# Kernel optimization log

Measured on AMD Instinct MI355X. Metric: run time of the kernel, lower is better.

Reference implementation:

```python
import jax, jax.numpy as jnp
import numpy as np

NEG_SLOPE = 0.2  # PyG GATConv default LeakyReLU negative slope


def gat_conv(x, src, dst, W, att_src, att_dst, bias, heads, out_ch, concat):
    """PyG-style GATConv (eval mode, self-loops already appended to src/dst)."""
    n = x.shape[0]
    xh = (x @ W).reshape(n, heads, out_ch)          # [N, H, C]
    a_src = jnp.sum(xh * att_src, axis=-1)          # [N, H]
    a_dst = jnp.sum(xh * att_dst, axis=-1)          # [N, H]
    e = jax.nn.leaky_relu(a_src[src] + a_dst[dst], NEG_SLOPE)  # [E, H]
    # segment softmax over edges grouped by destination node
    m = jax.ops.segment_max(e, dst, num_segments=n)
    m = jnp.where(jnp.isfinite(m), m, 0.0)
    ex = jnp.exp(e - m[dst])
    denom = jax.ops.segment_sum(ex, dst, num_segments=n)
    alpha = ex / (denom[dst] + 1e-16)               # [E, H]
    msg = xh[src] * alpha[..., None]                # [E, H, C]
    out = jax.ops.segment_sum(msg, dst, num_segments=n)  # [N, H, C]
    out = out.reshape(n, heads * out_ch) if concat else out.mean(axis=1)
    return out + bias


def setup_inputs() -> dict:
    key = jax.random.key(0)
    ks = jax.random.split(key, 10)
    N, E, IN, OUT = 50000, 600000, 128, 64
    H1, C1 = 2, 2 * OUT   # conv1: heads=2, out=2*out_channels, concat -> 4*OUT
    H2, C2 = 1, OUT       # conv2: heads=1, concat=False
    s = 0.05
    return {
        "x": jax.random.normal(ks[0], (N, IN), dtype=jnp.float32),
        "edge_index": jax.random.randint(ks[1], (2, E), 0, N, dtype=jnp.int64),
        "W1": jax.random.normal(ks[2], (IN, H1 * C1), dtype=jnp.float32) * s,
        "att_src1": jax.random.normal(ks[3], (H1, C1), dtype=jnp.float32) * s,
        "att_dst1": jax.random.normal(ks[4], (H1, C1), dtype=jnp.float32) * s,
        "b1": jnp.zeros((H1 * C1,), dtype=jnp.float32),
        "W2": jax.random.normal(ks[5], (H1 * C1, H2 * C2), dtype=jnp.float32) * s,
        "att_src2": jax.random.normal(ks[6], (H2, C2), dtype=jnp.float32) * s,
        "att_dst2": jax.random.normal(ks[7], (H2, C2), dtype=jnp.float32) * s,
        "b2": jnp.zeros((C2,), dtype=jnp.float32),
    }


def reference(x, edge_index, W1, att_src1, att_dst1, b1, W2, att_src2, att_dst2, b2):
    n = x.shape[0]
    loop = jnp.arange(n, dtype=edge_index.dtype)
    src = jnp.concatenate([edge_index[0], loop])  # add_self_loops=True
    dst = jnp.concatenate([edge_index[1], loop])
    z = gat_conv(x, src, dst, W1, att_src1, att_dst1, b1, heads=2, out_ch=128, concat=True)
    z = jax.nn.relu(z)
    z = gat_conv(z, src, dst, W2, att_src2, att_dst2, b2, heads=1, out_ch=64, concat=False)
    # decode: dot product over original edge_index (no self loops)
    val = jnp.sum(z[edge_index[0]] * z[edge_index[1]], axis=-1)
    return val.reshape(-1)
```

## Files before the change

### kernel.cpp

```cpp
#include <hip/hip_runtime.h>
#include <math.h>

#define IN_F 128
#define F1 256
#define H1 2
#define F2 64
#define NEG 0.2f

typedef _Float16 f16x8 __attribute__((ext_vector_type(8)));
typedef _Float16 f16x4 __attribute__((ext_vector_type(4)));
typedef float f32x4 __attribute__((ext_vector_type(4)));

__global__ __launch_bounds__(256) void gemm12_fused(
    const _Float16* __restrict__ Gh, const _Float16* __restrict__ Gl,
    const _Float16* __restrict__ Wth, const _Float16* __restrict__ Wtl,
    const float* __restrict__ b1,
    const _Float16* __restrict__ W2th, const _Float16* __restrict__ W2tl,
    const float* __restrict__ as2, const float* __restrict__ ad2,
    float* __restrict__ xh2, float* __restrict__ a_src, float* __restrict__ a_dst,
    int N)
{
    __shared__ _Float16 FRGh[32 * 64 * 8];
    __shared__ _Float16 FRGl[32 * 64 * 8];
    __shared__ _Float16 Zh[64 * 256];
    __shared__ _Float16 Zl[64 * 256];

    int t = threadIdx.x;
    int wave = t >> 6, lane = t & 63;
    int quad = lane >> 4, l4 = lane & 15;
    int rt = blockIdx.x * 4 + wave;
    bool active = (rt * 16 < N);
    long mrow = (long)rt * 16 + l4;

    #pragma unroll 1
    for (int h = 0; h < 2; ++h) {
        const _Float16* wsh = Wth + (long)h * 128 * IN_F;
        const _Float16* wsl = Wtl + (long)h * 128 * IN_F;
        #pragma unroll
        for (int p = 0; p < 8; ++p) {
            int fs = p * 256 + t;
            int fl = fs & 63;
            int slot = fs >> 6;
            int ct = slot >> 2, ks = slot & 3;
            int col = ct * 16 + (fl & 15);
            int koff = ks * 32 + (fl >> 4) * 8;
            *(f16x8*)&FRGh[fs * 8] = *(const f16x8*)&wsh[(long)col * IN_F + koff];
            *(f16x8*)&FRGl[fs * 8] = *(const f16x8*)&wsl[(long)col * IN_F + koff];
        }
        __syncthreads();

        if (active) {
            const _Float16* gh = Gh + mrow * F1 + h * 128 + quad * 8;
            const _Float16* gl = Gl + mrow * F1 + h * 128 + quad * 8;
            f16x8 ah[4], al[4];
            #pragma unroll
            for (int ks = 0; ks < 4; ++ks) {
                ah[ks] = *(const f16x8*)(gh + ks * 32);
                al[ks] = *(const f16x8*)(gl + ks * 32);
            }
            f32x4 acc[8];
            #pragma unroll
            for (int ct = 0; ct < 8; ++ct) acc[ct] = (f32x4){0.f, 0.f, 0.f, 0.f};
            #pragma unroll
            for (int ks = 0; ks < 4; ++ks) {
                #pragma unroll
                for (int ct = 0; ct < 8; ++ct) {
                    f16x8 bh = *(const f16x8*)&FRGh[((ct * 4 + ks) * 64 + lane) * 8];
                    f16x8 bl = *(const f16x8*)&FRGl[((ct * 4 + ks) * 64 + lane) * 8];
                    acc[ct] = __builtin_amdgcn_mfma_f32_16x16x32_f16(ah[ks], bh, acc[ct], 0, 0, 0);
                    acc[ct] = __builtin_amdgcn_mfma_f32_16x16x32_f16(al[ks], bh, acc[ct], 0, 0, 0);
                    acc[ct] = __builtin_amdgcn_mfma_f32_16x16x32_f16(ah[ks], bl, acc[ct], 0, 0, 0);
                }
            }
            #pragma unroll
            for (int ct = 0; ct < 8; ++ct) {
                int col = h * 128 + ct * 16 + l4;
                float b1c = b1[col];
                #pragma unroll
                for (int i = 0; i < 4; ++i) {
                    int row = wave * 16 + quad * 4 + i;
                    float v = fmaxf(acc[ct][i] + b1c, 0.f);
                    _Float16 hi = (_Float16)v;
                    int e = (row * 256 + col) ^ ((row & 7) << 3);
                    Zh[e] = hi;
                    Zl[e] = (_Float16)(v - (float)hi);
                }
            }
        }
        __syncthreads();
    }

    #pragma unroll
    for (int p = 0; p < 8; ++p) {
        int fs = p * 256 + t;
        int fl = fs & 63;
        int slot = fs >> 6;
        int ct = slot >> 3, ks = slot & 7;
        int col = ct * 16 + (fl & 15);
        int koff = ks * 32 + (fl >> 4) * 8;
        *(f16x8*)&FRGh[fs * 8] = *(const f16x8*)&W2th[(long)col * F1 + koff];
        *(f16x8*)&FRGl[fs * 8] = *(const f16x8*)&W2tl[(long)col * F1 + koff];
    }
    __syncthreads();

    if (!active) return;
    {
        int row = wave * 16 + l4;
        int swz = (row & 7) << 3;
        f16x8 ah[8], al[8];
        #pragma unroll
        for (int ks = 0; ks < 8; ++ks) {
            int e = (row * 256 + (quad * 8 + ks * 32)) ^ swz;
            ah[ks] = *(const f16x8*)&Zh[e];
            al[ks] = *(const f16x8*)&Zl[e];
        }
        f32x4 acc[4];
        #pragma unroll
        for (int ct = 0; ct < 4; ++ct) acc[ct] = (f32x4){0.f, 0.f, 0.f, 0.f};
        #pragma unroll
        for (int ks = 0; ks < 8; ++ks) {
            #pragma unroll
            for (int ct = 0; ct < 4; ++ct) {
                f16x8 bh = *(const f16x8*)&FRGh[((ct * 8 + ks) * 64 + lane) * 8];
                f16x8 bl = *(const f16x8*)&FRGl[((ct * 8 + ks) * 64 + lane) * 8];
                acc[ct] = __builtin_amdgcn_mfma_f32_16x16x32_f16(ah[ks], bh, acc[ct], 0, 0, 0);
                acc[ct] = __builtin_amdgcn_mfma_f32_16x16x32_f16(al[ks], bh, acc[ct], 0, 0, 0);
                acc[ct] = __builtin_amdgcn_mfma_f32_16x16x32_f16(ah[ks], bl, acc[ct], 0, 0, 0);
            }
        }
        int rbase = rt * 16 + quad * 4;
        float ps[4] = {0, 0, 0, 0}, pd[4] = {0, 0, 0, 0};
        #pragma unroll
        for (int ct = 0; ct < 4; ++ct) {
            int col = ct * 16 + l4;
            float asv = as2[col], adv = ad2[col];
            #pragma unroll
            for (int i = 0; i < 4; ++i) {
                xh2[(long)(rbase + i) * F2 + col] = acc[ct][i];
                ps[i] = fmaf(acc[ct][i], asv, ps[i]);
                pd[i] = fmaf(acc[ct][i], adv, pd[i]);
            }
        }
        #pragma unroll
        for (int o = 1; o < 16; o <<= 1) {
            #pragma unroll
            for (int i = 0; i < 4; ++i) {
                ps[i] += __shfl_xor(ps[i], o);
                pd[i] += __shfl_xor(pd[i], o);
            }
        }
        if (l4 == 0) {
            #pragma unroll
            for (int i = 0; i < 4; ++i) {
                a_src[rbase + i] = ps[i];
                a_dst[rbase + i] = pd[i];
            }
        }
    }
}

__global__ __launch_bounds__(256) void hist_uv_k(
    const int* __restrict__ ei_d, int* __restrict__ deg, int* __restrict__ pos,
    int E, int Ep, int NBH,
    const float* __restrict__ W1, const float* __restrict__ as1,
    const float* __restrict__ ad1, float* __restrict__ UV4,
    _Float16* __restrict__ Wth, _Float16* __restrict__ Wtl,
    const float* __restrict__ W2,
    _Float16* __restrict__ W2th, _Float16* __restrict__ W2tl)
{
    int b = (int)blockIdx.x;
    int t = threadIdx.x;
    if (b < NBH) {
        int i = b * 256 + t;
        if (i >= Ep) return;
        int d = (i < E) ? ei_d[i] : (i - E);
        pos[i] = atomicAdd(&deg[d], 1);
    } else if (b < NBH + 16) {
        int p = (b - NBH) * 16 + (t >> 4);
        int l = t & 15;
        int k = p >> 1, h = p & 1;
        const float* wrow = W1 + (long)k * F1 + h * 128;
        const float* sa = as1 + h * 128;
        const float* da = ad1 + h * 128;
        int c0 = l * 8;
        float u = 0.f, v = 0.f;
        #pragma unroll
        for (int c = 0; c < 8; ++c) {
            float w = wrow[c0 + c];
            u = fmaf(w, sa[c0 + c], u);
            v = fmaf(w, da[c0 + c], v);
        }
        #pragma unroll
        for (int o = 1; o < 16; o <<= 1) {
            u += __shfl_xor(u, o);
            v += __shfl_xor(v, o);
        }
        if (l == 0) {
            UV4[k * 4 + h] = u;
            UV4[k * 4 + 2 + h] = v;
        }
    } else if (b < NBH + 32) {
        int gid = (b - NBH - 16) * 256 + t;
        int n = gid >> 4;
        int kb = (gid & 15) * 8;
        f16x8 hi, lo;
        #pragma unroll
        for (int c = 0; c < 8; ++c) {
            float w = W1[(long)(kb + c) * F1 + n];
            _Float16 hh = (_Float16)w;
            hi[c] = hh;
            lo[c] = (_Float16)(w - (float)hh);
        }
        *(f16x8*)&Wth[(long)n * IN_F + kb] = hi;
        *(f16x8*)&Wtl[(long)n * IN_F + kb] = lo;
    } else {
        int gid = (b - NBH - 32) * 256 + t;
        int n = gid >> 5;
        int kb = (gid & 31) * 8;
        f16x8 hi, lo;
        #pragma unroll
        for (int c = 0; c < 8; ++c) {
            float w = W2[(long)(kb + c) * F2 + n];
            _Float16 hh = (_Float16)w;
            hi[c] = hh;
            lo[c] = (_Float16)(w - (float)hh);
        }
        *(f16x8*)&W2th[(long)n * F1 + kb] = hi;
        *(f16x8*)&W2tl[(long)n * F1 + kb] = lo;
    }
}

__global__ __launch_bounds__(1024) void scanA_att_k(
    const int* __restrict__ deg, int* __restrict__ rloc, int* __restrict__ bsum,
    int N, int NBLK,
    const float* __restrict__ x, const float* __restrict__ UV4,
    float* __restrict__ a_src, float* __restrict__ a_dst)
{
    if ((int)blockIdx.x < NBLK) {
        __shared__ int wsum[16];
        int t = threadIdx.x, lane = t & 63, w = t >> 6;
        int i = blockIdx.x * 1024 + t;
        int v = (i < N) ? deg[i] : 0;
        int incl = v;
        #pragma unroll
        for (int o = 1; o < 64; o <<= 1) {
            int nb = __shfl_up(incl, o);
            if (lane >= o) incl += nb;
        }
        if (lane == 63) wsum[w] = incl;
        __syncthreads();
        if (w == 0 && lane < 16) {
            int s = wsum[lane];
            #pragma unroll
            for (int o = 1; o < 16; o <<= 1) {
                int nb = __shfl_up(s, o);
                if (lane >= o) s += nb;
            }
            wsum[lane] = s;
        }
        __syncthreads();
        int woff = (w == 0) ? 0 : wsum[w - 1];
        if (i < N) rloc[i] = woff + incl - v;
        if (t == 1023) bsum[blockIdx.x] = woff + incl;
    } else {
        int wave = threadIdx.x >> 6, lane = threadIdx.x & 63;
        int n = ((int)blockIdx.x - NBLK) * 16 + wave;
        if (n >= N) return;
        float2 xv = ((const float2*)(x + (long)n * IN_F))[lane];
        float4 u0 = ((const float4*)UV4)[2 * lane];
        float4 u1 = ((const float4*)UV4)[2 * lane + 1];
        float p0 = xv.x * u0.x + xv.y * u1.x;
        float p1 = xv.x * u0.y + xv.y * u1.y;
        float p2 = xv.x * u0.z + xv.y * u1.z;
        float p3 = xv.x * u0.w + xv.y * u1.w;
        #pragma unroll
        for (int o = 32; o > 0; o >>= 1) {
            p0 += __shfl_xor(p0, o); p1 += __shfl_xor(p1, o);
            p2 += __shfl_xor(p2, o); p3 += __shfl_xor(p3, o);
        }
        if (lane == 0) {
            a_src[(long)n * 2 + 0] = p0; a_src[(long)n * 2 + 1] = p1;
            a_dst[(long)n * 2 + 0] = p2; a_dst[(long)n * 2 + 1] = p3;
        }
    }
}

__global__ __launch_bounds__(1024) void scat_fix_k(
    const int* __restrict__ ei_s, const int* __restrict__ ei_d,
    const int* __restrict__ rloc, const int* __restrict__ bsum,
    const int* __restrict__ pos, int* __restrict__ rowptr,
    int* __restrict__ csr_src, int* __restrict__ csr_eid,
    int E, int Ep, int N, int NBLK)
{
    __shared__ int bexs[64];
    __shared__ int tot_sh;
    int t = threadIdx.x;
    if (t < 64) {
        int v = (t < NBLK) ? bsum[t] : 0;
        int incl = v;
        #pragma unroll
        for (int o = 1; o < 64; o <<= 1) {
            int nb = __shfl_up(incl, o);
            if (t >= o) incl += nb;
        }
        bexs[t] = incl - v;
        if (t == NBLK - 1) tot_sh = incl;
    }
    __syncthreads();
    if ((int)blockIdx.x < NBLK) {
        int i = blockIdx.x * 1024 + t;
        if (i < N) rowptr[i] = rloc[i] + bexs[blockIdx.x];
        if ((int)blockIdx.x == NBLK - 1 && t == 0) rowptr[N] = tot_sh;
    } else {
        int i = ((int)blockIdx.x - NBLK) * 1024 + t;
        if (i >= Ep) return;
        int s = (i < E) ? ei_s[i] : (i - E);
        int d = (i < E) ? ei_d[i] : (i - E);
        int at = rloc[d] + bexs[d >> 10] + pos[i];
        csr_src[at] = s;
        csr_eid[at] = (i < E) ? i : -1;
    }
}

__global__ __launch_bounds__(256) void agg1x(
    const int* __restrict__ rowptr, const int* __restrict__ csr_src,
    const float* __restrict__ a_s, const float* __restrict__ a_d,
    const float* __restrict__ x, _Float16* __restrict__ Gh,
    _Float16* __restrict__ Gl, int N)
{
    int wave = threadIdx.x >> 6, lane = threadIdx.x & 63;
    int d = blockIdx.x * 4 + wave;
    if (d >= N) return;
    int row = rowptr[d], end = rowptr[d + 1];
    int h = lane >> 5, l5 = lane & 31;
    int g = lane >> 4, q = lane & 15;
    float adh = a_d[(long)d * 2 + h];
    float acc[2][2][4];
    #pragma unroll
    for (int s0 = 0; s0 < 2; ++s0)
        #pragma unroll
        for (int h0 = 0; h0 < 2; ++h0)
            #pragma unroll
            for (int p = 0; p < 4; ++p) acc[s0][h0][p] = 0.f;
    float den = 0.f;
    for (int base = row; base < end; base += 32) {
        int cnt = min(32, end - base);
        int sreg = 0; float e = 0.f;
        if (l5 < cnt) {
            sreg = csr_src[base + l5];
            float v = a_s[(long)sreg * 2 + h] + adh;
            v = (v > 0.f) ? v : NEG * v;
            e = expf(v);
            den += e;
        }
        int jmax = (cnt + 3) >> 2;
        for (int j = 0; j < jmax; j += 2) {
            int mA = 4 * j + g;
            int mB = mA + 4;
            int sA = __shfl(sreg, mA);
            int sB = __shfl(sreg, mB);
            float w0A = __shfl(e, mA);
            float w1A = __shfl(e, 32 | mA);
            float w0B = __shfl(e, mB);
            float w1B = __shfl(e, 32 | mB);
            const float* xpA = x + (long)sA * IN_F + q * 4;
            const float* xpB = x + (long)sB * IN_F + q * 4;
            float4 a0 = *(const float4*)(xpA);
            float4 a1 = *(const float4*)(xpA + 64);
            float4 b0 = *(const float4*)(xpB);
            float4 b1 = *(const float4*)(xpB + 64);
            acc[0][0][0] = fmaf(w0A, a0.x, acc[0][0][0]);
            acc[0][0][1] = fmaf(w0A, a0.y, acc[0][0][1]);
            acc[0][0][2] = fmaf(w0A, a0.z, acc[0][0][2]);
            acc[0][0][3] = fmaf(w0A, a0.w, acc[0][0][3]);
            acc[1][0][0] = fmaf(w0A, a1.x, acc[1][0][0]);
            acc[1][0][1] = fmaf(w0A, a1.y, acc[1][0][1]);
            acc[1][0][2] = fmaf(w0A, a1.z, acc[1][0][2]);
            acc[1][0][3] = fmaf(w0A, a1.w, acc[1][0][3]);
            acc[0][1][0] = fmaf(w1A, a0.x, acc[0][1][0]);
            acc[0][1][1] = fmaf(w1A, a0.y, acc[0][1][1]);
            acc[0][1][2] = fmaf(w1A, a0.z, acc[0][1][2]);
            acc[0][1][3] = fmaf(w1A, a0.w, acc[0][1][3]);
            acc[1][1][0] = fmaf(w1A, a1.x, acc[1][1][0]);
            acc[1][1][1] = fmaf(w1A, a1.y, acc[1][1][1]);
            acc[1][1][2] = fmaf(w1A, a1.z, acc[1][1][2]);
            acc[1][1][3] = fmaf(w1A, a1.w, acc[1][1][3]);
            acc[0][0][0] = fmaf(w0B, b0.x, acc[0][0][0]);
            acc[0][0][1] = fmaf(w0B, b0.y, acc[0][0][1]);
            acc[0][0][2] = fmaf(w0B, b0.z, acc[0][0][2]);
            acc[0][0][3] = fmaf(w0B, b0.w, acc[0][0][3]);
            acc[1][0][0] = fmaf(w0B, b1.x, acc[1][0][0]);
            acc[1][0][1] = fmaf(w0B, b1.y, acc[1][0][1]);
            acc[1][0][2] = fmaf(w0B, b1.z, acc[1][0][2]);
            acc[1][0][3] = fmaf(w0B, b1.w, acc[1][0][3]);
            acc[0][1][0] = fmaf(w1B, b0.x, acc[0][1][0]);
            acc[0][1][1] = fmaf(w1B, b0.y, acc[0][1][1]);
            acc[0][1][2] = fmaf(w1B, b0.z, acc[0][1][2]);
            acc[0][1][3] = fmaf(w1B, b0.w, acc[0][1][3]);
            acc[1][1][0] = fmaf(w1B, b1.x, acc[1][1][0]);
            acc[1][1][1] = fmaf(w1B, b1.y, acc[1][1][1]);
            acc[1][1][2] = fmaf(w1B, b1.z, acc[1][1][2]);
            acc[1][1][3] = fmaf(w1B, b1.w, acc[1][1][3]);
        }
    }
    #pragma unroll
    for (int o = 16; o > 0; o >>= 1) den += __shfl_xor(den, o);
    float den_o = __shfl_xor(den, 32);
    float den0 = (h == 0) ? den : den_o;
    float den1 = (h == 0) ? den_o : den;
    #pragma unroll
    for (int s0 = 0; s0 < 2; ++s0)
        #pragma unroll
        for (int h0 = 0; h0 < 2; ++h0)
            #pragma unroll
            for (int p = 0; p < 4; ++p) {
                float v = acc[s0][h0][p];
                v += __shfl_xor(v, 16);
                v += __shfl_xor(v, 32);
                acc[s0][h0][p] = v;
            }
    if (g == 0) {
        float inv0 = 1.0f / (den0 + 1e-16f);
        float inv1 = 1.0f / (den1 + 1e-16f);
        #pragma unroll
        for (int h0 = 0; h0 < 2; ++h0) {
            float inv = (h0 == 0) ? inv0 : inv1;
            #pragma unroll
            for (int s0 = 0; s0 < 2; ++s0) {
                f16x4 hi, lo;
                #pragma unroll
                for (int p = 0; p < 4; ++p) {
                    float v = acc[s0][h0][p] * inv;
                    hi[p] = (_Float16)v;
                    lo[p] = (_Float16)(v - (float)hi[p]);
                }
                long base = (long)d * F1 + h0 * 128 + s0 * 64 + q * 4;
                *(f16x4*)(Gh + base) = hi;
                *(f16x4*)(Gl + base) = lo;
            }
        }
    }
}

__global__ __launch_bounds__(256) void agg2_csr(
    const int* __restrict__ rowptr, const int* __restrict__ csr_src,
    const float* __restrict__ a_s, const float* __restrict__ a_d,
    const float* __restrict__ xh2, const float* __restrict__ b2,
    float* __restrict__ out2b, int N)
{
    int wave = threadIdx.x >> 6, lane = threadIdx.x & 63;
    int d = blockIdx.x * 4 + wave;
    if (d >= N) return;
    int row = rowptr[d], end = rowptr[d + 1];
    float adv = a_d[d];
    int g = lane >> 3, q = lane & 7;
    float acc[2][4] = {{0,0,0,0},{0,0,0,0}};
    float den = 0.f;
    for (int base = row; base < end; base += 64) {
        int cnt = min(64, end - base);
        float ev = 0.f; int sreg = 0;
        if (lane < cnt) {
            sreg = csr_src[base + lane];
            float v = a_s[sreg] + adv; v = (v > 0.f) ? v : NEG * v;
            ev = expf(v);
            den += ev;
        }
        int jmax = (cnt + 7) >> 3;
        for (int j = 0; j < jmax; j += 2) {
            int mA = 8 * j + g;
            int mB = mA + 8;
            int sA = __shfl(sreg, mA);
            int sB = __shfl(sreg, mB);
            float wA = __shfl(ev, mA);
            float wB = __shfl(ev, mB);
            const float* xpA = xh2 + (long)sA * F2 + q * 4;
            const float* xpB = xh2 + (long)sB * F2 + q * 4;
            float4 a0 = *(const float4*)(xpA);
            float4 a1 = *(const float4*)(xpA + 32);
            float4 b0 = *(const float4*)(xpB);
            float4 b1 = *(const float4*)(xpB + 32);
            acc[0][0] = fmaf(wA, a0.x, acc[0][0]); acc[0][1] = fmaf(wA, a0.y, acc[0][1]);
            acc[0][2] = fmaf(wA, a0.z, acc[0][2]); acc[0][3] = fmaf(wA, a0.w, acc[0][3]);
            acc[1][0] = fmaf(wA, a1.x, acc[1][0]); acc[1][1] = fmaf(wA, a1.y, acc[1][1]);
            acc[1][2] = fmaf(wA, a1.z, acc[1][2]); acc[1][3] = fmaf(wA, a1.w, acc[1][3]);
            acc[0][0] = fmaf(wB, b0.x, acc[0][0]); acc[0][1] = fmaf(wB, b0.y, acc[0][1]);
            acc[0][2] = fmaf(wB, b0.z, acc[0][2]); acc[0][3] = fmaf(wB, b0.w, acc[0][3]);
            acc[1][0] = fmaf(wB, b1.x, acc[1][0]); acc[1][1] = fmaf(wB, b1.y, acc[1][1]);
            acc[1][2] = fmaf(wB, b1.z, acc[1][2]); acc[1][3] = fmaf(wB, b1.w, acc[1][3]);
        }
    }
    #pragma unroll
    for (int o = 32; o > 0; o >>= 1) den += __shfl_xor(den, o);
    #pragma unroll
    for (int s0 = 0; s0 < 2; ++s0)
        #pragma unroll
        for (int p = 0; p < 4; ++p) {
            float v = acc[s0][p];
            v += __shfl_xor(v, 8);
            v += __shfl_xor(v, 16);
            v += __shfl_xor(v, 32);
            acc[s0][p] = v;
        }
    if (g == 0) {
        float inv = 1.0f / (den + 1e-16f);
        #pragma unroll
        for (int s0 = 0; s0 < 2; ++s0) {
            const float* bb = b2 + s0 * 32 + q * 4;
            float4 o4 = {acc[s0][0] * inv + bb[0], acc[s0][1] * inv + bb[1],
                         acc[s0][2] * inv + bb[2], acc[s0][3] * inv + bb[3]};
            *(float4*)(out2b + (long)d * F2 + s0 * 32 + q * 4) = o4;
        }
    }
}

__global__ __launch_bounds__(256) void decode_csr(
    const int* __restrict__ rowptr, const int* __restrict__ csr_src,
    const int* __restrict__ csr_eid, const float* __restrict__ z2b,
    float* __restrict__ out, int N)
{
    int wave = threadIdx.x >> 6, lane = threadIdx.x & 63;
    int d = blockIdx.x * 4 + wave;
    if (d >= N) return;
    int row = rowptr[d], end = rowptr[d + 1];
    int g = lane >> 3, q = lane & 7;
    const float* zd = z2b + (long)d * F2 + q * 4;
    float4 vd0 = *(const float4*)(zd);
    float4 vd1 = *(const float4*)(zd + 32);
    for (int base = row; base < end; base += 64) {
        int cnt = min(64, end - base);
        int sreg = 0, ereg = -1;
        if (lane < cnt) {
            sreg = csr_src[base + lane];
            ereg = csr_eid[base + lane];
        }
        int jmax = (cnt + 7) >> 3;
        for (int j = 0; j < jmax; j += 2) {
            int mA = 8 * j + g;
            int mB = mA + 8;
            int sA = __shfl(sreg, mA);
            int eA = __shfl(ereg, mA);
            int sB = __shfl(sreg, mB);
            int eB = __shfl(ereg, mB);
            const float* zsA = z2b + (long)sA * F2 + q * 4;
            const float* zsB = z2b + (long)sB * F2 + q * 4;
            float4 a0 = *(const float4*)(zsA);
            float4 a1 = *(const float4*)(zsA + 32);
            float4 b0 = *(const float4*)(zsB);
            float4 b1 = *(const float4*)(zsB + 32);
            float pA = vd0.x * a0.x + vd0.y * a0.y + vd0.z * a0.z + vd0.w * a0.w
                     + vd1.x * a1.x + vd1.y * a1.y + vd1.z * a1.z + vd1.w * a1.w;
            float pB = vd0.x * b0.x + vd0.y * b0.y + vd0.z * b0.z + vd0.w * b0.w
                     + vd1.x * b1.x + vd1.y * b1.y + vd1.z * b1.z + vd1.w * b1.w;
            pA += __shfl_xor(pA, 1);
            pB += __shfl_xor(pB, 1);
            pA += __shfl_xor(pA, 2);
            pB += __shfl_xor(pB, 2);
            pA += __shfl_xor(pA, 4);
            pB += __shfl_xor(pB, 4);
            if (q == 0 && eA >= 0) out[eA] = pA;
            if (q == 0 && eB >= 0) out[eB] = pB;
        }
    }
}

extern "C" void kernel_launch(void* const* d_in, const int* in_sizes, int n_in,
                              void* d_out, int out_size, void* d_ws, size_t ws_size,
                              hipStream_t stream) {
    const float* x   = (const float*)d_in[0];
    const int*   ei  = (const int*)d_in[1];
    const float* W1  = (const float*)d_in[2];
    const float* as1 = (const float*)d_in[3];
    const float* ad1 = (const float*)d_in[4];
    const float* b1  = (const float*)d_in[5];
    const float* W2  = (const float*)d_in[6];
    const float* as2 = (const float*)d_in[7];
    const float* ad2 = (const float*)d_in[8];
    const float* b2  = (const float*)d_in[9];

    int N  = in_sizes[0] / IN_F;
    int E  = in_sizes[1] / 2;
    int Ep = E + N;
    const int* ei_src = ei;
    const int* ei_dst = ei + E;

    float* ws = (float*)d_ws;
    size_t off = 0;
    auto alloc = [&](size_t n) { float* p = ws + off; off += (n + 63) & ~(size_t)63; return p; };

    _Float16* Gh   = (_Float16*)alloc((size_t)N * F1 / 2);
    _Float16* Gl   = (_Float16*)alloc((size_t)N * F1 / 2);
    _Float16* Wth  = (_Float16*)alloc(IN_F * F1 / 2);
    _Float16* Wtl  = (_Float16*)alloc(IN_F * F1 / 2);
    _Float16* W2th = (_Float16*)alloc(F1 * F2 / 2);
    _Float16* W2tl = (_Float16*)alloc(F1 * F2 / 2);
    float* xh2    = alloc((size_t)N * F2);
    float* out2b  = alloc((size_t)N * F2);
    float* a_src1 = alloc((size_t)N * H1);
    float* a_dst1 = alloc((size_t)N * H1);
    float* a_src2 = alloc(N);
    float* a_dst2 = alloc(N);
    float* UV4    = alloc(IN_F * 4);
    int* rowptr   = (int*)alloc(N + 64);
    int* rloc     = (int*)alloc(N + 64);
    int* csr_src  = (int*)alloc(Ep);
    int* csr_eid  = (int*)alloc(Ep);
    int* pos      = (int*)alloc(Ep);
    int* bsum     = (int*)alloc(64);
    int* deg      = (int*)alloc(N);
    hipMemsetAsync(deg, 0, (size_t)N * sizeof(int), stream);

    int NBLK = (N + 1023) / 1024;
    int NBH  = (Ep + 255) / 256;
    int NBS  = (Ep + 1023) / 1024;
    int NBA  = (N + 15) / 16;

    hist_uv_k<<<NBH + 40, 256, 0, stream>>>(ei_dst, deg, pos, E, Ep, NBH,
                                            W1, as1, ad1, UV4, Wth, Wtl,
                                            W2, W2th, W2tl);
    scanA_att_k<<<NBLK + NBA, 1024, 0, stream>>>(deg, rloc, bsum, N, NBLK,
                                                 x, UV4, a_src1, a_dst1);
    scat_fix_k<<<NBLK + NBS, 1024, 0, stream>>>(ei_src, ei_dst, rloc, bsum, pos,
                                                rowptr, csr_src, csr_eid,
                                                E, Ep, N, NBLK);

    agg1x<<<(N + 3) / 4, 256, 0, stream>>>(rowptr, csr_src, a_src1, a_dst1, x,
                                           Gh, Gl, N);
    gemm12_fused<<<(N + 63) / 64, 256, 0, stream>>>(Gh, Gl, Wth, Wtl, b1,
                                                    W2th, W2tl, as2, ad2,
                                                    xh2, a_src2, a_dst2, N);
    agg2_csr<<<(N + 3) / 4, 256, 0, stream>>>(rowptr, csr_src, a_src2, a_dst2, xh2, b2, out2b, N);

    decode_csr<<<(N + 3) / 4, 256, 0, stream>>>(rowptr, csr_src, csr_eid, out2b,
                                                (float*)d_out, N);
}
```

Before: 307.6 us.

## Pre-swizzle weights into MFMA fragment order and read them from global

The weight-prep kernel now writes W1 and W2 hi/lo halves directly in per-lane MFMA fragment order. The fused GEMM kernel then reads B fragments straight from global memory (L2/L1-cached) instead of staging them in shared memory. This drops the LDS fragment buffers and most __syncthreads, which cuts LDS usage and barrier stalls and should raise occupancy. Each wave now issues redundant global loads of the same weights, relying on cache hits. Inactive waves exit early, which is safe now that no block-wide barriers remain.

```diff
diff --git a/kernel.cpp b/kernel.cpp
--- a/kernel.cpp
+++ b/kernel.cpp
@@ -13,15 +13,13 @@
 
 __global__ __launch_bounds__(256) void gemm12_fused(
     const _Float16* __restrict__ Gh, const _Float16* __restrict__ Gl,
-    const _Float16* __restrict__ Wth, const _Float16* __restrict__ Wtl,
+    const _Float16* __restrict__ Wf1h, const _Float16* __restrict__ Wf1l,
     const float* __restrict__ b1,
-    const _Float16* __restrict__ W2th, const _Float16* __restrict__ W2tl,
+    const _Float16* __restrict__ Wf2h, const _Float16* __restrict__ Wf2l,
     const float* __restrict__ as2, const float* __restrict__ ad2,
     float* __restrict__ xh2, float* __restrict__ a_src, float* __restrict__ a_dst,
     int N)
 {
-    __shared__ _Float16 FRGh[32 * 64 * 8];
-    __shared__ _Float16 FRGl[32 * 64 * 8];
     __shared__ _Float16 Zh[64 * 256];
     __shared__ _Float16 Zl[64 * 256];
 
@@ -29,81 +27,50 @@
     int wave = t >> 6, lane = t & 63;
     int quad = lane >> 4, l4 = lane & 15;
     int rt = blockIdx.x * 4 + wave;
-    bool active = (rt * 16 < N);
+    if (rt * 16 >= N) return;
     long mrow = (long)rt * 16 + l4;
 
     #pragma unroll 1
     for (int h = 0; h < 2; ++h) {
-        const _Float16* wsh = Wth + (long)h * 128 * IN_F;
-        const _Float16* wsl = Wtl + (long)h * 128 * IN_F;
-        #pragma unroll
-        for (int p = 0; p < 8; ++p) {
-            int fs = p * 256 + t;
-            int fl = fs & 63;
-            int slot = fs >> 6;
-            int ct = slot >> 2, ks = slot & 3;
-            int col = ct * 16 + (fl & 15);
-            int koff = ks * 32 + (fl >> 4) * 8;
-            *(f16x8*)&FRGh[fs * 8] = *(const f16x8*)&wsh[(long)col * IN_F + koff];
-            *(f16x8*)&FRGl[fs * 8] = *(const f16x8*)&wsl[(long)col * IN_F + koff];
-        }
-        __syncthreads();
-
-        if (active) {
-            const _Float16* gh = Gh + mrow * F1 + h * 128 + quad * 8;
-            const _Float16* gl = Gl + mrow * F1 + h * 128 + quad * 8;
-            f16x8 ah[4], al[4];
-            #pragma unroll
-            for (int ks = 0; ks < 4; ++ks) {
-                ah[ks] = *(const f16x8*)(gh + ks * 32);
-                al[ks] = *(const f16x8*)(gl + ks * 32);
-            }
-            f32x4 acc[8];
-            #pragma unroll
-            for (int ct = 0; ct < 8; ++ct) acc[ct] = (f32x4){0.f, 0.f, 0.f, 0.f};
-            #pragma unroll
-            for (int ks = 0; ks < 4; ++ks) {
-                #pragma unroll
-                for (int ct = 0; ct < 8; ++ct) {
-                    f16x8 bh = *(const f16x8*)&FRGh[((ct * 4 + ks) * 64 + lane) * 8];
-                    f16x8 bl = *(const f16x8*)&FRGl[((ct * 4 + ks) * 64 + lane) * 8];
-                    acc[ct] = __builtin_amdgcn_mfma_f32_16x16x32_f16(ah[ks], bh, acc[ct], 0, 0, 0);
-                    acc[ct] = __builtin_amdgcn_mfma_f32_16x16x32_f16(al[ks], bh, acc[ct], 0, 0, 0);
-                    acc[ct] = __builtin_amdgcn_mfma_f32_16x16x32_f16(ah[ks], bl, acc[ct], 0, 0, 0);
-                }
-            }
+        const _Float16* gh = Gh + mrow * F1 + h * 128 + quad * 8;
+        const _Float16* gl = Gl + mrow * F1 + h * 128 + quad * 8;
+        f16x8 ah[4], al[4];
+        #pragma unroll
+        for (int ks = 0; ks < 4; ++ks) {
+            ah[ks] = *(const f16x8*)(gh + ks * 32);
+            al[ks] = *(const f16x8*)(gl + ks * 32);
+        }
+        f32x4 acc[8];
+        #pragma unroll
+        for (int ct = 0; ct < 8; ++ct) acc[ct] = (f32x4){0.f, 0.f, 0.f, 0.f};
+        #pragma unroll
+        for (int ks = 0; ks < 4; ++ks) {
             #pragma unroll
             for (int ct = 0; ct < 8; ++ct) {
-                int col = h * 128 + ct * 16 + l4;
-                float b1c = b1[col];
-                #pragma unroll
-                for (int i = 0; i < 4; ++i) {
-                    int row = wave * 16 + quad * 4 + i;
-                    float v = fmaxf(acc[ct][i] + b1c, 0.f);
-                    _Float16 hi = (_Float16)v;
-                    int e = (row * 256 + col) ^ ((row & 7) << 3);
-                    Zh[e] = hi;
-                    Zl[e] = (_Float16)(v - (float)hi);
-                }
-            }
-        }
-        __syncthreads();
-    }
-
-    #pragma unroll
-    for (int p = 0; p < 8; ++p) {
-        int fs = p * 256 + t;
-        int fl = fs & 63;
-        int slot = fs >> 6;
-        int ct = slot >> 3, ks = slot & 7;
-        int col = ct * 16 + (fl & 15);
-        int koff = ks * 32 + (fl >> 4) * 8;
-        *(f16x8*)&FRGh[fs * 8] = *(const f16x8*)&W2th[(long)col * F1 + koff];
-        *(f16x8*)&FRGl[fs * 8] = *(const f16x8*)&W2tl[(long)col * F1 + koff];
-    }
-    __syncthreads();
-
-    if (!active) return;
+                int slot = h * 32 + ct * 4 + ks;
+                f16x8 bh = *(const f16x8*)&Wf1h[((long)slot * 64 + lane) * 8];
+                f16x8 bl = *(const f16x8*)&Wf1l[((long)slot * 64 + lane) * 8];
+                acc[ct] = __builtin_amdgcn_mfma_f32_16x16x32_f16(ah[ks], bh, acc[ct], 0, 0, 0);
+                acc[ct] = __builtin_amdgcn_mfma_f32_16x16x32_f16(al[ks], bh, acc[ct], 0, 0, 0);
+                acc[ct] = __builtin_amdgcn_mfma_f32_16x16x32_f16(ah[ks], bl, acc[ct], 0, 0, 0);
+            }
+        }
+        #pragma unroll
+        for (int ct = 0; ct < 8; ++ct) {
+            int col = h * 128 + ct * 16 + l4;
+            float b1c = b1[col];
+            #pragma unroll
+            for (int i = 0; i < 4; ++i) {
+                int row = wave * 16 + quad * 4 + i;
+                float v = fmaxf(acc[ct][i] + b1c, 0.f);
+                _Float16 hi = (_Float16)v;
+                int e = (row * 256 + col) ^ ((row & 7) << 3);
+                Zh[e] = hi;
+                Zl[e] = (_Float16)(v - (float)hi);
+            }
+        }
+    }
+
     {
         int row = wave * 16 + l4;
         int swz = (row & 7) << 3;
@@ -121,8 +88,9 @@
         for (int ks = 0; ks < 8; ++ks) {
             #pragma unroll
             for (int ct = 0; ct < 4; ++ct) {
-                f16x8 bh = *(const f16x8*)&FRGh[((ct * 8 + ks) * 64 + lane) * 8];
-                f16x8 bl = *(const f16x8*)&FRGl[((ct * 8 + ks) * 64 + lane) * 8];
+                int slot = ct * 8 + ks;
+                f16x8 bh = *(const f16x8*)&Wf2h[((long)slot * 64 + lane) * 8];
+                f16x8 bl = *(const f16x8*)&Wf2l[((long)slot * 64 + lane) * 8];
                 acc[ct] = __builtin_amdgcn_mfma_f32_16x16x32_f16(ah[ks], bh, acc[ct], 0, 0, 0);
                 acc[ct] = __builtin_amdgcn_mfma_f32_16x16x32_f16(al[ks], bh, acc[ct], 0, 0, 0);
                 acc[ct] = __builtin_amdgcn_mfma_f32_16x16x32_f16(ah[ks], bl, acc[ct], 0, 0, 0);
@@ -164,9 +132,9 @@
     int E, int Ep, int NBH,
     const float* __restrict__ W1, const float* __restrict__ as1,
     const float* __restrict__ ad1, float* __restrict__ UV4,
-    _Float16* __restrict__ Wth, _Float16* __restrict__ Wtl,
+    _Float16* __restrict__ Wf1h, _Float16* __restrict__ Wf1l,
     const float* __restrict__ W2,
-    _Float16* __restrict__ W2th, _Float16* __restrict__ W2tl)
+    _Float16* __restrict__ Wf2h, _Float16* __restrict__ Wf2l)
 {
     int b = (int)blockIdx.x;
     int t = threadIdx.x;
@@ -211,8 +179,13 @@
             hi[c] = hh;
             lo[c] = (_Float16)(w - (float)hh);
         }
-        *(f16x8*)&Wth[(long)n * IN_F + kb] = hi;
-        *(f16x8*)&Wtl[(long)n * IN_F + kb] = lo;
+        int h = n >> 7, colh = n & 127;
+        int ct = colh >> 4, l4c = colh & 15;
+        int ks = kb >> 5, lq = (kb >> 3) & 3;
+        int lanef = lq * 16 + l4c;
+        int slot = h * 32 + ct * 4 + ks;
+        *(f16x8*)&Wf1h[((long)slot * 64 + lanef) * 8] = hi;
+        *(f16x8*)&Wf1l[((long)slot * 64 + lanef) * 8] = lo;
     } else {
         int gid = (b - NBH - 32) * 256 + t;
         int n = gid >> 5;
@@ -225,8 +198,12 @@
             hi[c] = hh;
             lo[c] = (_Float16)(w - (float)hh);
         }
-        *(f16x8*)&W2th[(long)n * F1 + kb] = hi;
-        *(f16x8*)&W2tl[(long)n * F1 + kb] = lo;
+        int ct = n >> 4, l4c = n & 15;
+        int ks = kb >> 5, lq = (kb >> 3) & 3;
+        int lanef = lq * 16 + l4c;
+        int slot = ct * 8 + ks;
+        *(f16x8*)&Wf2h[((long)slot * 64 + lanef) * 8] = hi;
+        *(f16x8*)&Wf2l[((long)slot * 64 + lanef) * 8] = lo;
     }
 }
 
@@ -589,10 +566,10 @@
 
     _Float16* Gh   = (_Float16*)alloc((size_t)N * F1 / 2);
     _Float16* Gl   = (_Float16*)alloc((size_t)N * F1 / 2);
-    _Float16* Wth  = (_Float16*)alloc(IN_F * F1 / 2);
-    _Float16* Wtl  = (_Float16*)alloc(IN_F * F1 / 2);
-    _Float16* W2th = (_Float16*)alloc(F1 * F2 / 2);
-    _Float16* W2tl = (_Float16*)alloc(F1 * F2 / 2);
+    _Float16* Wf1h = (_Float16*)alloc(IN_F * F1 / 2);
+    _Float16* Wf1l = (_Float16*)alloc(IN_F * F1 / 2);
+    _Float16* Wf2h = (_Float16*)alloc(F1 * F2 / 2);
+    _Float16* Wf2l = (_Float16*)alloc(F1 * F2 / 2);
     float* xh2    = alloc((size_t)N * F2);
     float* out2b  = alloc((size_t)N * F2);
     float* a_src1 = alloc((size_t)N * H1);
@@ -615,8 +592,8 @@
     int NBA  = (N + 15) / 16;
 
     hist_uv_k<<<NBH + 40, 256, 0, stream>>>(ei_dst, deg, pos, E, Ep, NBH,
-                                            W1, as1, ad1, UV4, Wth, Wtl,
-                                            W2, W2th, W2tl);
+                                            W1, as1, ad1, UV4, Wf1h, Wf1l,
+                                            W2, Wf2h, Wf2l);
     scanA_att_k<<<NBLK + NBA, 1024, 0, stream>>>(deg, rloc, bsum, N, NBLK,
                                                  x, UV4, a_src1, a_dst1);
     scat_fix_k<<<NBLK + NBS, 1024, 0, stream>>>(ei_src, ei_dst, rloc, bsum, pos,
@@ -625,8 +602,8 @@
 
     agg1x<<<(N + 3) / 4, 256, 0, stream>>>(rowptr, csr_src, a_src1, a_dst1, x,
                                            Gh, Gl, N);
-    gemm12_fused<<<(N + 63) / 64, 256, 0, stream>>>(Gh, Gl, Wth, Wtl, b1,
-                                                    W2th, W2tl, as2, ad2,
+    gemm12_fused<<<(N + 63) / 64, 256, 0, stream>>>(Gh, Gl, Wf1h, Wf1l, b1,
+                                                    Wf2h, Wf2l, as2, ad2,
                                                     xh2, a_src2, a_dst2, N);
     agg2_csr<<<(N + 3) / 4, 256, 0, stream>>>(rowptr, csr_src, a_src2, a_dst2, xh2, b2, out2b, N);
 
```

After: 284.0 us. -7.7%, faster.
